# Kernel optimization log

Measured on AMD Instinct MI355X. Metric: run time of the kernel, lower is better.

## Reference

```python
import jax, jax.numpy as jnp
import numpy as np


def _lstm_seq(x, W, U, b, reverse):
    """Run an LSTM over time. x: [B,T,F], W: [F,4H], U: [H,4H], b: [4H].
    Returns hidden states [B,T,H]. reverse=True mimics go_backwards + output
    reversal (lax.scan(reverse=True) stores outputs at their original index).
    Keras gate order: i, f, c(g), o; sigmoid recurrent activation, tanh activation."""
    B, T, F = x.shape
    H = U.shape[0]
    # Precompute input projections for all timesteps (one big GEMM).
    xz = jnp.einsum('btf,fg->btg', x, W) + b  # [B,T,4H]

    def step(carry, xz_t):
        h, c = carry
        z = xz_t + h @ U  # [B,4H]
        i, f, g, o = jnp.split(z, 4, axis=-1)
        i = jax.nn.sigmoid(i)
        f = jax.nn.sigmoid(f)
        g = jnp.tanh(g)
        o = jax.nn.sigmoid(o)
        c = f * c + i * g
        h = o * jnp.tanh(c)
        return (h, c), h

    init = (jnp.zeros((B, H), x.dtype), jnp.zeros((B, H), x.dtype))
    _, hs = jax.lax.scan(step, init, jnp.swapaxes(xz, 0, 1), reverse=reverse)
    return jnp.swapaxes(hs, 0, 1)  # [B,T,H]


def setup_inputs() -> dict:
    key = jax.random.key(0)
    ks = jax.random.split(key, 7)
    B, T, F, H = 128, 2048, 128, 8
    s = lambda *sh: 1.0 / np.sqrt(sh[0])
    return {
        'x': jax.random.normal(ks[0], (B, T, F), jnp.float32),
        'W_fw': jax.random.normal(ks[1], (F, 4 * H), jnp.float32) * s(F),
        'U_fw': jax.random.normal(ks[2], (H, 4 * H), jnp.float32) * s(H),
        'b_fw': jax.random.normal(ks[3], (4 * H,), jnp.float32) * 0.1,
        'W_bw': jax.random.normal(ks[4], (F, 4 * H), jnp.float32) * s(F),
        'U_bw': jax.random.normal(ks[5], (H, 4 * H), jnp.float32) * s(H),
        'b_bw': jax.random.normal(ks[6], (4 * H,), jnp.float32) * 0.1,
    }


def reference(x, W_fw, U_fw, b_fw, W_bw, U_bw, b_bw):
    out_fw = _lstm_seq(x, W_fw, U_fw, b_fw, reverse=False)
    out_bw = _lstm_seq(x, W_bw, U_bw, b_bw, reverse=True)  # already time-aligned
    return jnp.concatenate([out_fw, out_bw], axis=-1)  # [B,T,2H]
```

## Files before the change

kernel.cpp:

```cpp
#include <hip/hip_runtime.h>

#define LOG2E 1.44269504088896340736f

constexpr int B  = 128;
constexpr int T  = 2048;
constexpr int Fd = 128;
constexpr int H  = 8;
constexpr int BT = B * T;


__global__ __launch_bounds__(256) void lstm_proj(
    const float* __restrict__ x,
    const float* __restrict__ W_fw, const float* __restrict__ b_fw,
    const float* __restrict__ W_bw, const float* __restrict__ b_bw,
    float* __restrict__ xz)
{
    __shared__ float Wl[Fd * 64];
    __shared__ float Xs[64 * Fd];

    const int tid = threadIdx.x;
    for (int i = tid; i < Fd * 64; i += 256) {
        int f = i >> 6, q = i & 63;
        int d = q >> 5, pos = q & 31;
        int u = pos >> 1, ph = pos & 1;
        float sc = (ph == 0) ? (-LOG2E) : ((u < 8) ? (-2.0f * LOG2E) : (-LOG2E));
        const float* Wd = d ? W_bw : W_fw;
        Wl[i] = Wd[f * 32 + ph * 16 + u] * sc;
    }

    const int gg = tid & 15;
    const int rg = tid >> 4;
    const int d  = gg >> 3;
    const int p0 = (gg & 7) * 4;

    float bq[4];
    #pragma unroll
    for (int q = 0; q < 4; ++q) {
        int pos = p0 + q, u = pos >> 1, ph = pos & 1;
        float sc = (ph == 0) ? (-LOG2E) : ((u < 8) ? (-2.0f * LOG2E) : (-LOG2E));
        bq[q] = (d ? b_bw : b_fw)[ph * 16 + u] * sc;
    }

    for (int sub = 0; sub < 4; ++sub) {
        const int rbase = blockIdx.x * 256 + sub * 64;
        const float* src = x + (size_t)rbase * Fd;
        #pragma unroll
        for (int k = 0; k < 8; ++k) {
            int g = tid + k * 256;
            __builtin_amdgcn_global_load_lds(
                (const __attribute__((address_space(1))) void*)(src + g * 4),
                (__attribute__((address_space(3))) void*)(&Xs[g * 4]),
                16, 0, 0);
        }
        __syncthreads();

        float acc[4][4];
        #pragma unroll
        for (int r = 0; r < 4; ++r)
            #pragma unroll
            for (int q = 0; q < 4; ++q) acc[r][q] = 0.f;

        #pragma unroll 4
        for (int ff = 0; ff < Fd / 4; ++ff) {
            float4 xv[4];
            #pragma unroll
            for (int r = 0; r < 4; ++r)
                xv[r] = *(const float4*)(&Xs[(rg * 4 + r) * Fd + ff * 4]);
            #pragma unroll
            for (int i = 0; i < 4; ++i) {
                float4 w = *(const float4*)(&Wl[(ff * 4 + i) * 64 + d * 32 + p0]);
                #pragma unroll
                for (int r = 0; r < 4; ++r) {
                    float xf = (i == 0) ? xv[r].x : (i == 1) ? xv[r].y
                             : (i == 2) ? xv[r].z : xv[r].w;
                    acc[r][0] = fmaf(xf, w.x, acc[r][0]);
                    acc[r][1] = fmaf(xf, w.y, acc[r][1]);
                    acc[r][2] = fmaf(xf, w.z, acc[r][2]);
                    acc[r][3] = fmaf(xf, w.w, acc[r][3]);
                }
            }
        }

        const int row0 = rbase + rg * 4;
        const int t0 = row0 & 2047;
        const int bb = row0 >> 11;
        const size_t sbase = (size_t)(bb * 2 + d) * 65536;
        if (d == 0) {
            float* dst = xz + sbase + (size_t)(t0 >> 3) * 256 + (t0 & 7);
            #pragma unroll
            for (int q = 0; q < 4; ++q)
                *(float4*)(dst + (p0 + q) * 8) = make_float4(
                    acc[0][q] + bq[q], acc[1][q] + bq[q],
                    acc[2][q] + bq[q], acc[3][q] + bq[q]);
        } else {
            const int trow0 = 2047 - t0;
            float* dst = xz + sbase + (size_t)(trow0 >> 3) * 256 + ((trow0 & 7) - 3);
            #pragma unroll
            for (int q = 0; q < 4; ++q)
                *(float4*)(dst + (p0 + q) * 8) = make_float4(
                    acc[3][q] + bq[q], acc[2][q] + bq[q],
                    acc[1][q] + bq[q], acc[0][q] + bq[q]);
        }
        __syncthreads();
    }
}


#define ROT(X, R) __int_as_float(__builtin_amdgcn_update_dpp(                \
                      0, __float_as_int(X), 0x120 + R, 0xf, 0xf, false))
#define DPPSEL(X, MASK) __int_as_float(__builtin_amdgcn_update_dpp(          \
                      __float_as_int(X), __float_as_int(X), 0x128, 0xf, MASK, false))

__global__ __launch_bounds__(64) void lstm_scan(
    const float* __restrict__ xz,
    const float* __restrict__ U_fw,
    const float* __restrict__ U_bw,
    float* __restrict__ out)
{
    const int lane = threadIdx.x;
    const int rl   = lane & 15;
    const int task = blockIdx.x * 4 + (lane >> 4);
    const int s    = task & 255;
    const int c    = task >> 8;
    const int b    = s >> 1;
    const int dir  = s & 1;
    const int j    = rl & 7;
    const bool low = (rl < 8);

    const float* U = dir ? U_bw : U_fw;

    const float sA = -LOG2E;
    const float sB = low ? (-2.0f * LOG2E) : (-LOG2E);

    float uA0, uA1, uA2, uA3, uA4, uA5, uA6, uA7;
    float uB0, uB1, uB2, uB3, uB4, uB5, uB6, uB7;
    uA0 = U[j * 32 + rl] * sA;
    uB0 = U[j * 32 + 16 + rl] * sB;
#define PROBE(R) {                                                            \
        int rec = __builtin_amdgcn_update_dpp(0, rl + 1, 0x120 + R, 0xf, 0xf, false); \
        int sj  = (rec - 1) & 7;                                              \
        uA##R = U[sj * 32 + rl]      * sA;                                    \
        uB##R = U[sj * 32 + 16 + rl] * sB; }
    PROBE(1) PROBE(2) PROBE(3) PROBE(4) PROBE(5) PROBE(6) PROBE(7)
#undef PROBE

    const int wg = (c * 8 < 12) ? c * 8 : 12;
    const int g0 = c * 8 - wg;
    const float* gp = xz + (size_t)s * 65536 + (size_t)g0 * 256 + rl * 16;

    const int ue = c * 64;
    float* sp = out + ((size_t)b * T + (dir ? (2047 - ue) : ue)) * (2 * H)
              + dir * H + j;
    const int sdelta = dir ? -(2 * H) : (2 * H);

    float h = 0.f, c0 = 0.f;
    float m1 = 0.f, m2 = 0.f, m3 = 0.f, m4 = 0.f, m5 = 0.f, m6 = 0.f, m7 = 0.f;

#define STEP(ZA, ZB, ST) {                                                    \
        float a0 = fmaf(h,  uA0, (ZA));                                       \
        float a1 = m1 * uA1, a2 = m2 * uA2, a3 = m3 * uA3;                    \
        a0 = fmaf(m4, uA4, a0); a1 = fmaf(m5, uA5, a1);                       \
        a2 = fmaf(m6, uA6, a2); a3 = fmaf(m7, uA7, a3);                       \
        float zAf = (a0 + a1) + (a2 + a3);                                    \
        float b0 = fmaf(h,  uB0, (ZB));                                       \
        float b1 = m1 * uB1, b2 = m2 * uB2, b3 = m3 * uB3;                    \
        b0 = fmaf(m4, uB4, b0); b1 = fmaf(m5, uB5, b1);                       \
        b2 = fmaf(m6, uB6, b2); b3 = fmaf(m7, uB7, b3);                       \
        float zBf = (b0 + b1) + (b2 + b3);                                    \
        float eA = __builtin_amdgcn_exp2f(zAf);                               \
        float eB = __builtin_amdgcn_exp2f(zBf);                               \
        float aA = __builtin_amdgcn_rcpf(1.0f + eA);                          \
        float rB = __builtin_amdgcn_rcpf(1.0f + eB);                          \
        float q1 = aA * (-4.0f * LOG2E);                                      \
        float q2 = aA * ( 2.0f * LOG2E);                                      \
        float p  = fmaf(rB, q1, q2);                    \
        float pv  = DPPSEL(p,  0xc);                                          \
        float fco = DPPSEL(aA, 0x3);                                          \
        float oco = DPPSEL(rB, 0x3);                                          \
        c0 = fmaf(fco, c0, pv);                                               \
        float e2 = __builtin_amdgcn_exp2f(c0);                                \
        float r2 = __builtin_amdgcn_rcpf(1.0f + e2);                          \
        h = fmaf(r2, oco + oco, -oco);                                        \
        m1 = ROT(h, 1); m2 = ROT(h, 2); m3 = ROT(h, 3); m4 = ROT(h, 4);       \
        m5 = ROT(h, 5); m6 = ROT(h, 6); m7 = ROT(h, 7);                       \
        if (ST) { *sp = h; sp += sdelta; }                                    \
    }

#define STEPS8(A0, A1, B0, B1, ST)                                            \
        STEP(A0.x, B0.x, ST) STEP(A0.y, B0.y, ST) STEP(A0.z, B0.z, ST)        \
        STEP(A0.w, B0.w, ST) STEP(A1.x, B1.x, ST) STEP(A1.y, B1.y, ST)        \
        STEP(A1.z, B1.z, ST) STEP(A1.w, B1.w, ST)

    float4 A0, A1, B0, B1, NA0, NA1, NB0, NB1;
    A0 = *(const float4*)(gp + 0);
    A1 = *(const float4*)(gp + 4);
    B0 = *(const float4*)(gp + 8);
    B1 = *(const float4*)(gp + 12);

    for (int i = 0; i < wg; ++i) {
        NA0 = *(const float4*)(gp + 256); NA1 = *(const float4*)(gp + 260);
        NB0 = *(const float4*)(gp + 264); NB1 = *(const float4*)(gp + 268);
        STEPS8(A0, A1, B0, B1, 0)
        A0 = NA0; A1 = NA1; B0 = NB0; B1 = NB1;
        gp += 256;
    }
    for (int i = 0; i < 7; ++i) {
        NA0 = *(const float4*)(gp + 256); NA1 = *(const float4*)(gp + 260);
        NB0 = *(const float4*)(gp + 264); NB1 = *(const float4*)(gp + 268);
        STEPS8(A0, A1, B0, B1, 1)
        A0 = NA0; A1 = NA1; B0 = NB0; B1 = NB1;
        gp += 256;
    }
    STEPS8(A0, A1, B0, B1, 1)
#undef STEPS8
#undef STEP
}

extern "C" void kernel_launch(void* const* d_in, const int* in_sizes, int n_in,
                              void* d_out, int out_size, void* d_ws, size_t ws_size,
                              hipStream_t stream)
{
    const float* x    = (const float*)d_in[0];
    const float* W_fw = (const float*)d_in[1];
    const float* U_fw = (const float*)d_in[2];
    const float* b_fw = (const float*)d_in[3];
    const float* W_bw = (const float*)d_in[4];
    const float* U_bw = (const float*)d_in[5];
    const float* b_bw = (const float*)d_in[6];
    float* out = (float*)d_out;
    float* xz  = (float*)d_ws;

    lstm_proj<<<BT / 256, 256, 0, stream>>>(x, W_fw, b_fw, W_bw, b_bw, xz);
    lstm_scan<<<(2 * B * 32) / 4, 64, 0, stream>>>(xz, U_fw, U_bw, out);
}
```

Before: 132.0 us.

## Read x directly from global in projection GEMM with 8x8 register tiles

The projection kernel no longer stages x through shared memory with async global-to-LDS loads and sub-iterations. Each thread now loads its own 8 rows of x straight from global memory as float4 and computes an 8x8 register tile against the LDS-resident weights, writing two float4 per gate column. This removes the LDS staging and the per-subtile barriers and raises arithmetic per weight load, at the cost of more registers and uncoalesced per-thread global reads of x.

```diff
diff --git a/kernel.cpp b/kernel.cpp
--- a/kernel.cpp
+++ b/kernel.cpp
@@ -16,7 +16,6 @@
     float* __restrict__ xz)
 {
     __shared__ float Wl[Fd * 64];
-    __shared__ float Xs[64 * Fd];
 
     const int tid = threadIdx.x;
     for (int i = tid; i < Fd * 64; i += 256) {
@@ -27,81 +26,83 @@
         const float* Wd = d ? W_bw : W_fw;
         Wl[i] = Wd[f * 32 + ph * 16 + u] * sc;
     }
-
-    const int gg = tid & 15;
-    const int rg = tid >> 4;
-    const int d  = gg >> 3;
-    const int p0 = (gg & 7) * 4;
-
-    float bq[4];
+    __syncthreads();
+
+    const int gg = tid & 7;
+    const int rq = tid >> 3;
+    const int d  = gg >> 2;
+    const int p0 = (gg & 3) * 8;
+
+    float bq[8];
     #pragma unroll
-    for (int q = 0; q < 4; ++q) {
+    for (int q = 0; q < 8; ++q) {
         int pos = p0 + q, u = pos >> 1, ph = pos & 1;
         float sc = (ph == 0) ? (-LOG2E) : ((u < 8) ? (-2.0f * LOG2E) : (-LOG2E));
         bq[q] = (d ? b_bw : b_fw)[ph * 16 + u] * sc;
     }
 
-    for (int sub = 0; sub < 4; ++sub) {
-        const int rbase = blockIdx.x * 256 + sub * 64;
-        const float* src = x + (size_t)rbase * Fd;
-        #pragma unroll
-        for (int k = 0; k < 8; ++k) {
-            int g = tid + k * 256;
-            __builtin_amdgcn_global_load_lds(
-                (const __attribute__((address_space(1))) void*)(src + g * 4),
-                (__attribute__((address_space(3))) void*)(&Xs[g * 4]),
-                16, 0, 0);
-        }
-        __syncthreads();
-
-        float acc[4][4];
-        #pragma unroll
-        for (int r = 0; r < 4; ++r)
+    const int rbase = blockIdx.x * 256 + rq * 8;
+    const float* xp = x + (size_t)rbase * Fd;
+    const float* wbase = Wl + d * 32 + p0;
+
+    float acc[8][8];
+    #pragma unroll
+    for (int r = 0; r < 8; ++r)
+        #pragma unroll
+        for (int q = 0; q < 8; ++q) acc[r][q] = 0.f;
+
+    #pragma unroll 2
+    for (int kq = 0; kq < 32; ++kq) {
+        float4 xv[8];
+        #pragma unroll
+        for (int r = 0; r < 8; ++r)
+            xv[r] = *(const float4*)(xp + r * Fd + kq * 4);
+        #pragma unroll
+        for (int kk = 0; kk < 4; ++kk) {
+            float4 w0 = *(const float4*)(wbase + (kq * 4 + kk) * 64);
+            float4 w1 = *(const float4*)(wbase + (kq * 4 + kk) * 64 + 4);
             #pragma unroll
-            for (int q = 0; q < 4; ++q) acc[r][q] = 0.f;
-
-        #pragma unroll 4
-        for (int ff = 0; ff < Fd / 4; ++ff) {
-            float4 xv[4];
-            #pragma unroll
-            for (int r = 0; r < 4; ++r)
-                xv[r] = *(const float4*)(&Xs[(rg * 4 + r) * Fd + ff * 4]);
-            #pragma unroll
-            for (int i = 0; i < 4; ++i) {
-                float4 w = *(const float4*)(&Wl[(ff * 4 + i) * 64 + d * 32 + p0]);
-                #pragma unroll
-                for (int r = 0; r < 4; ++r) {
-                    float xf = (i == 0) ? xv[r].x : (i == 1) ? xv[r].y
-                             : (i == 2) ? xv[r].z : xv[r].w;
-                    acc[r][0] = fmaf(xf, w.x, acc[r][0]);
-                    acc[r][1] = fmaf(xf, w.y, acc[r][1]);
-                    acc[r][2] = fmaf(xf, w.z, acc[r][2]);
-                    acc[r][3] = fmaf(xf, w.w, acc[r][3]);
-                }
+            for (int r = 0; r < 8; ++r) {
+                float xf = (kk == 0) ? xv[r].x : (kk == 1) ? xv[r].y
+                         : (kk == 2) ? xv[r].z : xv[r].w;
+                acc[r][0] = fmaf(xf, w0.x, acc[r][0]);
+                acc[r][1] = fmaf(xf, w0.y, acc[r][1]);
+                acc[r][2] = fmaf(xf, w0.z, acc[r][2]);
+                acc[r][3] = fmaf(xf, w0.w, acc[r][3]);
+                acc[r][4] = fmaf(xf, w1.x, acc[r][4]);
+                acc[r][5] = fmaf(xf, w1.y, acc[r][5]);
+                acc[r][6] = fmaf(xf, w1.z, acc[r][6]);
+                acc[r][7] = fmaf(xf, w1.w, acc[r][7]);
             }
         }
-
-        const int row0 = rbase + rg * 4;
-        const int t0 = row0 & 2047;
-        const int bb = row0 >> 11;
-        const size_t sbase = (size_t)(bb * 2 + d) * 65536;
-        if (d == 0) {
-            float* dst = xz + sbase + (size_t)(t0 >> 3) * 256 + (t0 & 7);
-            #pragma unroll
-            for (int q = 0; q < 4; ++q)
-                *(float4*)(dst + (p0 + q) * 8) = make_float4(
-                    acc[0][q] + bq[q], acc[1][q] + bq[q],
-                    acc[2][q] + bq[q], acc[3][q] + bq[q]);
-        } else {
-            const int trow0 = 2047 - t0;
-            float* dst = xz + sbase + (size_t)(trow0 >> 3) * 256 + ((trow0 & 7) - 3);
-            #pragma unroll
-            for (int q = 0; q < 4; ++q)
-                *(float4*)(dst + (p0 + q) * 8) = make_float4(
-                    acc[3][q] + bq[q], acc[2][q] + bq[q],
-                    acc[1][q] + bq[q], acc[0][q] + bq[q]);
+    }
+
+    const int t0 = rbase & 2047;
+    const int bb = rbase >> 11;
+    const size_t sbase = (size_t)(bb * 2 + d) * 65536;
+    if (d == 0) {
+        float* dst = xz + sbase + (size_t)(t0 >> 3) * 256;
+        #pragma unroll
+        for (int q = 0; q < 8; ++q) {
+            *(float4*)(dst + (p0 + q) * 8) = make_float4(
+                acc[0][q] + bq[q], acc[1][q] + bq[q],
+                acc[2][q] + bq[q], acc[3][q] + bq[q]);
+            *(float4*)(dst + (p0 + q) * 8 + 4) = make_float4(
+                acc[4][q] + bq[q], acc[5][q] + bq[q],
+                acc[6][q] + bq[q], acc[7][q] + bq[q]);
         }
-        __syncthreads();
+    } else {
+        const int trow0 = 2047 - t0;
+        float* dst = xz + sbase + (size_t)(trow0 >> 3) * 256;
+        #pragma unroll
+        for (int q = 0; q < 8; ++q) {
+            *(float4*)(dst + (p0 + q) * 8) = make_float4(
+                acc[7][q] + bq[q], acc[6][q] + bq[q],
+                acc[5][q] + bq[q], acc[4][q] + bq[q]);
+            *(float4*)(dst + (p0 + q) * 8 + 4) = make_float4(
+                acc[3][q] + bq[q], acc[2][q] + bq[q],
+                acc[1][q] + bq[q], acc[0][q] + bq[q]);
+        }
     }
 }
 
```

New measurement: 149.9 us. +13.6%, slower.
